# Kernel optimization log

Hardware: AMD Instinct MI355X
Metric: run time of the kernel (lower is better)

## Reference

```python
import jax, jax.numpy as jnp
import numpy as np

D_MODEL = 1024
EPS_DT = 1e-4
LN_EPS = 1e-5


def _layernorm(y, gamma, beta):
    mu = jnp.mean(y, axis=-1, keepdims=True)
    var = jnp.var(y, axis=-1, keepdims=True)
    return (y - mu) * jax.lax.rsqrt(var + LN_EPS) * gamma + beta


def setup_inputs() -> dict:
    key = jax.random.key(0)
    ks = jax.random.split(key, 8)
    B, T, D = 8, 4096, D_MODEL
    s = 1.0 / np.sqrt(D)  # ~ torch Linear default init scale
    return {
        "x": jax.random.normal(ks[0], (B, T, D), jnp.float32),
        "delta_t": jax.random.uniform(ks[1], (B, T, D), jnp.float32),
        "log_decay": jnp.zeros((D,), jnp.float32),
        "W_in": jax.random.uniform(ks[2], (D, D), jnp.float32, -s, s),
        "b_in": jax.random.uniform(ks[3], (D,), jnp.float32, -s, s),
        "W_gate": jax.random.uniform(ks[4], (D, D), jnp.float32, -s, s),
        "b_gate": jax.random.uniform(ks[5], (D,), jnp.float32, -s, s),
        "W_out": jax.random.uniform(ks[6], (D, D), jnp.float32, -s, s),
        "b_out": jax.random.uniform(ks[7], (D,), jnp.float32, -s, s),
        "gamma": jnp.ones((D,), jnp.float32),
        "beta": jnp.zeros((D,), jnp.float32),
    }


def reference(x, delta_t, log_decay, W_in, b_in, W_gate, b_gate, W_out, b_out, gamma, beta):
    B, T, D = x.shape
    decay = jax.nn.softplus(log_decay) + 1e-4          # [D]
    dt = jnp.maximum(delta_t, EPS_DT)                   # [B,T,D]
    lamb = jnp.exp(-decay * dt)                         # [B,T,D]
    # Drive terms depend only on x -> precompute in parallel (big GEMMs).
    update = jnp.einsum('btd,ed->bte', x, W_in) + b_in
    gate = jax.nn.sigmoid(jnp.einsum('btd,ed->bte', x, W_gate) + b_gate)
    drive = (1.0 - lamb) * gate * update                # [B,T,D]

    def step(state, inputs):
        l_t, d_t = inputs
        state = l_t * state + d_t
        return state, state

    state0 = jnp.zeros((B, D), x.dtype)
    final_state, states = jax.lax.scan(
        step, state0,
        (jnp.swapaxes(lamb, 0, 1), jnp.swapaxes(drive, 0, 1)))
    states = jnp.swapaxes(states, 0, 1)                 # [B,T,D]
    # dropout is identity in eval mode
    y = states + jnp.einsum('btd,ed->bte', states, W_out) + b_out
    out = _layernorm(y, gamma, beta)
    return out, final_state
```

## Files before the change

### kernel.cpp

```cpp
#include <hip/hip_runtime.h>
#include <hip/hip_bf16.h>

#define D_MODEL 1024
#define BATCH 8
#define SEQ 4096
#define MROWS (BATCH*SEQ)
#define NC 64
#define CL 64

typedef __attribute__((ext_vector_type(4))) float f32x4;
typedef __attribute__((ext_vector_type(8))) short s16x8;

__device__ __forceinline__ unsigned short f2bf(float f){
  union { float f; unsigned int u; } v; v.f = f;
  return (unsigned short)((v.u + 0x7fffu + ((v.u >> 16) & 1u)) >> 16);
}
__device__ __forceinline__ float bf2f(unsigned int bits){
  union { unsigned int u; float f; } v; v.u = bits << 16; return v.f;
}

__device__ __forceinline__ void gload16(const void* g, void* l){
  __builtin_amdgcn_global_load_lds(
      (const __attribute__((address_space(1))) unsigned int*)g,
      (__attribute__((address_space(3))) unsigned int*)l, 16, 0, 0);
}

__global__ __launch_bounds__(256)
void prep_x_kernel(const float* __restrict__ x, unsigned short* __restrict__ xb, int n4){
  int i = blockIdx.x*256 + threadIdx.x;
  int stride = gridDim.x*256;
  for (; i < n4; i += stride){
    float4 v = ((const float4*)x)[i];
    ushort4 o;
    o.x = f2bf(v.x); o.y = f2bf(v.y); o.z = f2bf(v.z); o.w = f2bf(v.w);
    ((ushort4*)xb)[i] = o;
  }
}

__global__ __launch_bounds__(256)
void prep_w_kernel(const float* __restrict__ Wi, const float* __restrict__ Wg,
                   const float* __restrict__ Wo, const float* __restrict__ ld,
                   unsigned short* __restrict__ Wib, unsigned short* __restrict__ Wgb,
                   unsigned short* __restrict__ Wob, float* __restrict__ decay){
  int i = blockIdx.x*256 + threadIdx.x;
  {
    float4 a = ((const float4*)Wi)[i]; ushort4 o;
    o.x=f2bf(a.x); o.y=f2bf(a.y); o.z=f2bf(a.z); o.w=f2bf(a.w); ((ushort4*)Wib)[i]=o;
    a = ((const float4*)Wg)[i];
    o.x=f2bf(a.x); o.y=f2bf(a.y); o.z=f2bf(a.z); o.w=f2bf(a.w); ((ushort4*)Wgb)[i]=o;
    a = ((const float4*)Wo)[i];
    o.x=f2bf(a.x); o.y=f2bf(a.y); o.z=f2bf(a.z); o.w=f2bf(a.w); ((ushort4*)Wob)[i]=o;
  }
  if (i < D_MODEL){
    float v = ld[i];
    float sp = fmaxf(v, 0.f) + log1pf(expf(-fabsf(v)));
    decay[i] = sp + 1e-4f;
  }
}

__global__ __launch_bounds__(256, 3)
void gemm1_kernel(const unsigned short* __restrict__ Aglob,
                  const unsigned short* __restrict__ Bglob,
                  const float* __restrict__ bias,
                  unsigned short* __restrict__ Cout)
{
  __shared__ unsigned short sA[128*64];
  __shared__ unsigned short sB[128*64];
  const int tid  = threadIdx.x;
  const int lane = tid & 63;
  const int wave = tid >> 6;
  const int wr = wave >> 1, wc = wave & 1;
  const int bid = blockIdx.x;
  const int swz = ((bid & 7) << 8) | (bid >> 3);
  const int bcol = (swz & 7) * 128;
  const int brow = (swz >> 3) * 128;

  const f32x4 zero = {0.f,0.f,0.f,0.f};
  f32x4 acc[4][4];
  #pragma unroll
  for (int a=0;a<4;a++)
    #pragma unroll
    for (int b=0;b<4;b++) acc[a][b]=zero;

  for (int kt = 0; kt < D_MODEL/64; ++kt){
    __syncthreads();
    #pragma unroll
    for (int i=0;i<4;i++){
      const int ob = i*256 + wave*64;
      const int o  = ob + lane;
      const int r  = o >> 3;
      const int c  = ((o & 7) ^ (r & 7)) * 16;
      gload16((const char*)Aglob + (size_t)(brow + r)*(D_MODEL*2) + (size_t)kt*128 + c,
              (char*)sA + (size_t)ob*16);
      gload16((const char*)Bglob + (size_t)(bcol + r)*(D_MODEL*2) + (size_t)kt*128 + c,
              (char*)sB + (size_t)ob*16);
    }
    __syncthreads();
    #pragma unroll
    for (int ks=0; ks<2; ++ks){
      s16x8 af[4], bf[4];
      #pragma unroll
      for (int mi=0; mi<4; mi++){
        const int row = wr*64 + mi*16 + (lane & 15);
        const int chunk = (ks*4 + (lane>>4)) ^ (row & 7);
        af[mi] = *(const s16x8*)((const char*)sA + row*128 + chunk*16);
      }
      #pragma unroll
      for (int ni=0; ni<4; ni++){
        const int n = wc*64 + ni*16 + (lane & 15);
        const int chunk = (ks*4 + (lane>>4)) ^ (n & 7);
        bf[ni] = *(const s16x8*)((const char*)sB + n*128 + chunk*16);
      }
      #pragma unroll
      for (int mi=0; mi<4; mi++)
        #pragma unroll
        for (int ni=0; ni<4; ni++)
          acc[mi][ni] = __builtin_amdgcn_mfma_f32_16x16x32_bf16(af[mi], bf[ni], acc[mi][ni], 0,0,0);
    }
  }

  #pragma unroll
  for (int ni=0; ni<4; ni++){
    const int col = bcol + wc*64 + ni*16 + (lane & 15);
    const float vb = bias[col];
    #pragma unroll
    for (int mi=0; mi<4; mi++){
      #pragma unroll
      for (int q=0; q<4; q++){
        const int row = brow + wr*64 + mi*16 + ((lane>>4)*4) + q;
        Cout[(size_t)row*D_MODEL + col] = f2bf(acc[mi][ni][q] + vb);
      }
    }
  }
}

__global__ __launch_bounds__(256)
void scan_passA(const unsigned short* __restrict__ ub,
                const unsigned short* __restrict__ gb,
                const float* __restrict__ delta,
                const float* __restrict__ decay,
                unsigned int* __restrict__ pack,
                float* __restrict__ cA, float* __restrict__ cB){
  const int d0 = (blockIdx.x*256 + threadIdx.x)*2;
  const int c = blockIdx.y, b = blockIdx.z;
  const float dc0 = decay[d0], dc1 = decay[d0+1];
  size_t base = ((size_t)b*SEQ + (size_t)c*CL)*D_MODEL + d0;
  float A0=1.f, A1=1.f, s0=0.f, s1=0.f;
  #pragma unroll 4
  for (int t=0;t<CL;t++){
    const size_t idx = base + (size_t)t*D_MODEL;
    const unsigned int uu = *(const unsigned int*)(ub + idx);
    const unsigned int gg = *(const unsigned int*)(gb + idx);
    const float2 dv = *(const float2*)(delta + idx);
    const float u0 = bf2f(uu & 0xffffu), u1 = bf2f(uu >> 16);
    const float z0 = bf2f(gg & 0xffffu), z1 = bf2f(gg >> 16);
    const float g0 = 1.f/(1.f + __expf(-z0));
    const float g1 = 1.f/(1.f + __expf(-z1));
    const float lam0 = __expf(-dc0 * fmaxf(dv.x, 1e-4f));
    const float lam1 = __expf(-dc1 * fmaxf(dv.y, 1e-4f));
    const float om0 = 1.f - lam0, om1 = 1.f - lam1;
    const float dr0 = om0 * g0 * u0;
    const float dr1 = om1 * g1 * u1;
    uint2 pw;
    pw.x = ((unsigned int)f2bf(dr0) << 16) | (unsigned int)f2bf(om0);
    pw.y = ((unsigned int)f2bf(dr1) << 16) | (unsigned int)f2bf(om1);
    *(uint2*)(pack + idx) = pw;
    A0 *= lam0; A1 *= lam1;
    s0 = fmaf(lam0, s0, dr0);
    s1 = fmaf(lam1, s1, dr1);
  }
  const size_t ci = ((size_t)b*NC + c)*D_MODEL + d0;
  *(float2*)(cA+ci) = make_float2(A0,A1);
  *(float2*)(cB+ci) = make_float2(s0,s1);
}

__global__ __launch_bounds__(256)
void scan_passB(const float* __restrict__ cA, const float* __restrict__ cB,
                float* __restrict__ cS, float* __restrict__ fstate){
  const int d0 = (blockIdx.x*256 + threadIdx.x)*2;
  const int b = blockIdx.y;
  float s0=0.f, s1=0.f;
  for (int c=0;c<NC;c++){
    const size_t ci = ((size_t)b*NC + c)*D_MODEL + d0;
    *(float2*)(cS+ci) = make_float2(s0,s1);
    float2 a  = *(const float2*)(cA+ci);
    float2 bb = *(const float2*)(cB+ci);
    s0 = fmaf(a.x, s0, bb.x);
    s1 = fmaf(a.y, s1, bb.y);
  }
  *(float2*)(fstate + (size_t)b*D_MODEL + d0) = make_float2(s0,s1);
}

__global__ __launch_bounds__(256)
void scan_passC(const unsigned int* __restrict__ pack, const float* __restrict__ cS,
                unsigned short* __restrict__ statesb){
  const int d0 = (blockIdx.x*256 + threadIdx.x)*2;
  const int c = blockIdx.y, b = blockIdx.z;
  float2 sv = *(const float2*)(cS + ((size_t)b*NC + c)*D_MODEL + d0);
  float s0 = sv.x, s1 = sv.y;
  size_t base = ((size_t)b*SEQ + (size_t)c*CL)*D_MODEL + d0;
  #pragma unroll 8
  for (int t=0;t<CL;t++){
    uint2 p = *(const uint2*)(pack + base + (size_t)t*D_MODEL);
    float om0 = bf2f(p.x & 0xffffu), dr0 = bf2f(p.x >> 16);
    float om1 = bf2f(p.y & 0xffffu), dr1 = bf2f(p.y >> 16);
    s0 = fmaf(-om0, s0, s0) + dr0;
    s1 = fmaf(-om1, s1, s1) + dr1;
    unsigned int w = ((unsigned int)f2bf(s1) << 16) | (unsigned int)f2bf(s0);
    *(unsigned int*)(statesb + base + (size_t)t*D_MODEL) = w;
  }
}

__global__ __launch_bounds__(256)
void ln_kernel(const unsigned short* __restrict__ yb, const unsigned short* __restrict__ statesb,
               const float* __restrict__ gamma, const float* __restrict__ beta,
               float* __restrict__ out)
{
  const int row = blockIdx.x;
  const int tid = threadIdx.x;
  ushort4 yv = ((const ushort4*)(yb + (size_t)row*D_MODEL))[tid];
  ushort4 sb = ((const ushort4*)(statesb + (size_t)row*D_MODEL))[tid];
  float4 v;
  v.x = bf2f(yv.x) + bf2f(sb.x);
  v.y = bf2f(yv.y) + bf2f(sb.y);
  v.z = bf2f(yv.z) + bf2f(sb.z);
  v.w = bf2f(yv.w) + bf2f(sb.w);
  float s = v.x+v.y+v.z+v.w;
  float q = v.x*v.x + v.y*v.y + v.z*v.z + v.w*v.w;
  #pragma unroll
  for (int off=32; off>0; off>>=1){ s += __shfl_xor(s, off); q += __shfl_xor(q, off); }
  __shared__ float rs[4], rq[4];
  const int wave = tid>>6, lane = tid&63;
  if (lane==0){ rs[wave]=s; rq[wave]=q; }
  __syncthreads();
  float ts = rs[0]+rs[1]+rs[2]+rs[3];
  float tq = rq[0]+rq[1]+rq[2]+rq[3];
  float mu  = ts * (1.f/D_MODEL);
  float var = tq * (1.f/D_MODEL) - mu*mu;
  float inv = rsqrtf(var + 1e-5f);
  float4 g = ((const float4*)gamma)[tid];
  float4 b = ((const float4*)beta)[tid];
  float4 o;
  o.x = (v.x-mu)*inv*g.x + b.x;
  o.y = (v.y-mu)*inv*g.y + b.y;
  o.z = (v.z-mu)*inv*g.z + b.z;
  o.w = (v.w-mu)*inv*g.w + b.w;
  ((float4*)(out + (size_t)row*D_MODEL))[tid] = o;
}

extern "C" void kernel_launch(void* const* d_in, const int* in_sizes, int n_in,
                              void* d_out, int out_size, void* d_ws, size_t ws_size,
                              hipStream_t stream) {
  const float* x         = (const float*)d_in[0];
  const float* delta     = (const float*)d_in[1];
  const float* log_decay = (const float*)d_in[2];
  const float* W_in      = (const float*)d_in[3];
  const float* b_in      = (const float*)d_in[4];
  const float* W_gate    = (const float*)d_in[5];
  const float* b_gate    = (const float*)d_in[6];
  const float* W_out     = (const float*)d_in[7];
  const float* b_out     = (const float*)d_in[8];
  const float* gamma     = (const float*)d_in[9];
  const float* beta      = (const float*)d_in[10];

  char* w = (char*)d_ws;
  unsigned short* xb   = (unsigned short*)(w);
  unsigned short* Wib  = (unsigned short*)(w + 67108864);
  unsigned short* Wgb  = (unsigned short*)(w + 69206016);
  unsigned short* Wob  = (unsigned short*)(w + 71303168);
  float*          decay= (float*)        (w + 73400320);
  float*          cA   = (float*)        (w + 73404416);
  float*          cB   = (float*)        (w + 75501568);
  float*          cS   = (float*)        (w + 77598720);
  unsigned int*   pack = (unsigned int*) (w + 79695872);
  unsigned short* ybuf = (unsigned short*)pack;
  unsigned short* statesb = xb;

  float* out    = (float*)d_out;
  float* fstate = out + (size_t)MROWS*D_MODEL;
  unsigned short* ub = (unsigned short*)d_out;
  unsigned short* gb = ub + (size_t)MROWS*D_MODEL;

  hipLaunchKernelGGL(prep_x_kernel, dim3(8192), dim3(256), 0, stream, x, xb, MROWS*D_MODEL/4);
  hipLaunchKernelGGL(prep_w_kernel, dim3(1024), dim3(256), 0, stream,
                     W_in, W_gate, W_out, log_decay, Wib, Wgb, Wob, decay);
  hipLaunchKernelGGL(gemm1_kernel, dim3(2048), dim3(256), 0, stream, xb, Wib, b_in, ub);
  hipLaunchKernelGGL(gemm1_kernel, dim3(2048), dim3(256), 0, stream, xb, Wgb, b_gate, gb);
  hipLaunchKernelGGL(scan_passA, dim3(2,NC,BATCH), dim3(256), 0, stream,
                     ub, gb, delta, decay, pack, cA, cB);
  hipLaunchKernelGGL(scan_passB, dim3(2,BATCH), dim3(256), 0, stream, cA, cB, cS, fstate);
  hipLaunchKernelGGL(scan_passC, dim3(2,NC,BATCH), dim3(256), 0, stream, pack, cS, statesb);
  hipLaunchKernelGGL(gemm1_kernel, dim3(2048), dim3(256), 0, stream, statesb, Wob, b_out, ybuf);
  hipLaunchKernelGGL(ln_kernel, dim3(MROWS), dim3(256), 0, stream, ybuf, statesb, gamma, beta, out);
}
```

Baseline: 416.6 us.

## Fuse up/gate GEMMs, merge prep kernels, fold residual into output GEMM

Merges the x and weight conversion kernels into one launch and concatenates W_in and W_gate so one GEMM with doubled N produces both update and gate, sharing A-tile loads. The output GEMM adds the residual states in-register from the A tile already staged in shared memory, so the layernorm kernel no longer rereads the states buffer. This reduces launches and global traffic, at the cost of a conditional extra LDS pass inside the GEMM loop.

```diff
diff --git a/kernel.cpp b/kernel.cpp
--- a/kernel.cpp
+++ b/kernel.cpp
@@ -26,43 +26,45 @@
 }
 
 __global__ __launch_bounds__(256)
-void prep_x_kernel(const float* __restrict__ x, unsigned short* __restrict__ xb, int n4){
-  int i = blockIdx.x*256 + threadIdx.x;
-  int stride = gridDim.x*256;
-  for (; i < n4; i += stride){
-    float4 v = ((const float4*)x)[i];
-    ushort4 o;
-    o.x = f2bf(v.x); o.y = f2bf(v.y); o.z = f2bf(v.z); o.w = f2bf(v.w);
-    ((ushort4*)xb)[i] = o;
-  }
-}
-
-__global__ __launch_bounds__(256)
-void prep_w_kernel(const float* __restrict__ Wi, const float* __restrict__ Wg,
-                   const float* __restrict__ Wo, const float* __restrict__ ld,
-                   unsigned short* __restrict__ Wib, unsigned short* __restrict__ Wgb,
-                   unsigned short* __restrict__ Wob, float* __restrict__ decay){
-  int i = blockIdx.x*256 + threadIdx.x;
-  {
+void prep_all_kernel(const float* __restrict__ x,
+                     const float* __restrict__ Wi, const float* __restrict__ Wg,
+                     const float* __restrict__ Wo, const float* __restrict__ ld,
+                     unsigned short* __restrict__ xb,
+                     unsigned short* __restrict__ Wugb,
+                     unsigned short* __restrict__ Wob,
+                     float* __restrict__ decay, int nx4){
+  const int b = blockIdx.x;
+  if (b < 8192){
+    int i = b*256 + threadIdx.x;
+    for (; i < nx4; i += 8192*256){
+      float4 v = ((const float4*)x)[i];
+      ushort4 o;
+      o.x = f2bf(v.x); o.y = f2bf(v.y); o.z = f2bf(v.z); o.w = f2bf(v.w);
+      ((ushort4*)xb)[i] = o;
+    }
+  } else {
+    const int i = (b-8192)*256 + threadIdx.x;
     float4 a = ((const float4*)Wi)[i]; ushort4 o;
-    o.x=f2bf(a.x); o.y=f2bf(a.y); o.z=f2bf(a.z); o.w=f2bf(a.w); ((ushort4*)Wib)[i]=o;
+    o.x=f2bf(a.x); o.y=f2bf(a.y); o.z=f2bf(a.z); o.w=f2bf(a.w); ((ushort4*)Wugb)[i]=o;
     a = ((const float4*)Wg)[i];
-    o.x=f2bf(a.x); o.y=f2bf(a.y); o.z=f2bf(a.z); o.w=f2bf(a.w); ((ushort4*)Wgb)[i]=o;
+    o.x=f2bf(a.x); o.y=f2bf(a.y); o.z=f2bf(a.z); o.w=f2bf(a.w); ((ushort4*)Wugb)[i + D_MODEL*D_MODEL/4]=o;
     a = ((const float4*)Wo)[i];
     o.x=f2bf(a.x); o.y=f2bf(a.y); o.z=f2bf(a.z); o.w=f2bf(a.w); ((ushort4*)Wob)[i]=o;
-  }
-  if (i < D_MODEL){
-    float v = ld[i];
-    float sp = fmaxf(v, 0.f) + log1pf(expf(-fabsf(v)));
-    decay[i] = sp + 1e-4f;
+    if (i < D_MODEL){
+      float v = ld[i];
+      float sp = fmaxf(v, 0.f) + log1pf(expf(-fabsf(v)));
+      decay[i] = sp + 1e-4f;
+    }
   }
 }
 
 __global__ __launch_bounds__(256, 3)
-void gemm1_kernel(const unsigned short* __restrict__ Aglob,
-                  const unsigned short* __restrict__ Bglob,
-                  const float* __restrict__ bias,
-                  unsigned short* __restrict__ Cout)
+void gemm_ug_kernel(const unsigned short* __restrict__ Aglob,
+                    const unsigned short* __restrict__ Bglob,
+                    const float* __restrict__ b_in,
+                    const float* __restrict__ b_gate,
+                    unsigned short* __restrict__ ub,
+                    unsigned short* __restrict__ gb)
 {
   __shared__ unsigned short sA[128*64];
   __shared__ unsigned short sB[128*64];
@@ -70,10 +72,11 @@
   const int lane = tid & 63;
   const int wave = tid >> 6;
   const int wr = wave >> 1, wc = wave & 1;
-  const int bid = blockIdx.x;
-  const int swz = ((bid & 7) << 8) | (bid >> 3);
-  const int bcol = (swz & 7) * 128;
-  const int brow = (swz >> 3) * 128;
+  const int bid  = blockIdx.x;
+  const int idx  = bid >> 3;
+  const int xcd  = bid & 7;
+  const int bcol = (idx & 15) * 128;
+  const int brow = (xcd*32 + (idx >> 4)) * 128;
 
   const f32x4 zero = {0.f,0.f,0.f,0.f};
   f32x4 acc[4][4];
@@ -119,16 +122,20 @@
     }
   }
 
+  const int half = bcol >> 10;
+  const float* bias = half ? b_gate : b_in;
+  unsigned short* Co = half ? gb : ub;
+  const int cb = bcol & 1023;
   #pragma unroll
   for (int ni=0; ni<4; ni++){
-    const int col = bcol + wc*64 + ni*16 + (lane & 15);
+    const int col = cb + wc*64 + ni*16 + (lane & 15);
     const float vb = bias[col];
     #pragma unroll
     for (int mi=0; mi<4; mi++){
       #pragma unroll
       for (int q=0; q<4; q++){
         const int row = brow + wr*64 + mi*16 + ((lane>>4)*4) + q;
-        Cout[(size_t)row*D_MODEL + col] = f2bf(acc[mi][ni][q] + vb);
+        Co[(size_t)row*D_MODEL + col] = f2bf(acc[mi][ni][q] + vb);
       }
     }
   }
@@ -211,20 +218,109 @@
   }
 }
 
-__global__ __launch_bounds__(256)
-void ln_kernel(const unsigned short* __restrict__ yb, const unsigned short* __restrict__ statesb,
+__global__ __launch_bounds__(256, 3)
+void gemm_out_kernel(const unsigned short* __restrict__ Sb,
+                     const unsigned short* __restrict__ Wob,
+                     const float* __restrict__ b_out,
+                     unsigned short* __restrict__ yb)
+{
+  __shared__ unsigned short sA[128*64];
+  __shared__ unsigned short sB[128*64];
+  const int tid  = threadIdx.x;
+  const int lane = tid & 63;
+  const int wave = tid >> 6;
+  const int wr = wave >> 1, wc = wave & 1;
+  const int bid = blockIdx.x;
+  const int swz = ((bid & 7) << 8) | (bid >> 3);
+  const int bcol = (swz & 7) * 128;
+  const int brow = (swz >> 3) * 128;
+
+  const f32x4 zero = {0.f,0.f,0.f,0.f};
+  f32x4 acc[4][4];
+  #pragma unroll
+  for (int a=0;a<4;a++)
+    #pragma unroll
+    for (int b=0;b<4;b++) acc[a][b]=zero;
+
+  const int kt_res = (bcol >> 6) + wc;
+
+  for (int kt = 0; kt < D_MODEL/64; ++kt){
+    __syncthreads();
+    #pragma unroll
+    for (int i=0;i<4;i++){
+      const int ob = i*256 + wave*64;
+      const int o  = ob + lane;
+      const int r  = o >> 3;
+      const int c  = ((o & 7) ^ (r & 7)) * 16;
+      gload16((const char*)Sb  + (size_t)(brow + r)*(D_MODEL*2) + (size_t)kt*128 + c,
+              (char*)sA + (size_t)ob*16);
+      gload16((const char*)Wob + (size_t)(bcol + r)*(D_MODEL*2) + (size_t)kt*128 + c,
+              (char*)sB + (size_t)ob*16);
+    }
+    __syncthreads();
+    #pragma unroll
+    for (int ks=0; ks<2; ++ks){
+      s16x8 af[4], bf[4];
+      #pragma unroll
+      for (int mi=0; mi<4; mi++){
+        const int row = wr*64 + mi*16 + (lane & 15);
+        const int chunk = (ks*4 + (lane>>4)) ^ (row & 7);
+        af[mi] = *(const s16x8*)((const char*)sA + row*128 + chunk*16);
+      }
+      #pragma unroll
+      for (int ni=0; ni<4; ni++){
+        const int n = wc*64 + ni*16 + (lane & 15);
+        const int chunk = (ks*4 + (lane>>4)) ^ (n & 7);
+        bf[ni] = *(const s16x8*)((const char*)sB + n*128 + chunk*16);
+      }
+      #pragma unroll
+      for (int mi=0; mi<4; mi++)
+        #pragma unroll
+        for (int ni=0; ni<4; ni++)
+          acc[mi][ni] = __builtin_amdgcn_mfma_f32_16x16x32_bf16(af[mi], bf[ni], acc[mi][ni], 0,0,0);
+    }
+    if (kt == kt_res){
+      #pragma unroll
+      for (int ni=0; ni<4; ni++){
+        #pragma unroll
+        for (int mi=0; mi<4; mi++){
+          #pragma unroll
+          for (int q=0; q<4; q++){
+            const int rl = wr*64 + mi*16 + ((lane>>4)*4) + q;
+            const int cl = ni*16 + (lane & 15);
+            const int byte = rl*128 + (((cl>>3) ^ (rl&7))*16) + ((cl&7)*2);
+            acc[mi][ni][q] += bf2f((unsigned int)*(const unsigned short*)((const char*)sA + byte));
+          }
+        }
+      }
+    }
+  }
+
+  #pragma unroll
+  for (int ni=0; ni<4; ni++){
+    const int col = bcol + wc*64 + ni*16 + (lane & 15);
+    const float vb = b_out[col];
+    #pragma unroll
+    for (int mi=0; mi<4; mi++){
+      #pragma unroll
+      for (int q=0; q<4; q++){
+        const int row = brow + wr*64 + mi*16 + ((lane>>4)*4) + q;
+        yb[(size_t)row*D_MODEL + col] = f2bf(acc[mi][ni][q] + vb);
+      }
+    }
+  }
+}
+
+__global__ __launch_bounds__(256)
+void ln_kernel(const unsigned short* __restrict__ yb,
                const float* __restrict__ gamma, const float* __restrict__ beta,
                float* __restrict__ out)
 {
   const int row = blockIdx.x;
   const int tid = threadIdx.x;
   ushort4 yv = ((const ushort4*)(yb + (size_t)row*D_MODEL))[tid];
-  ushort4 sb = ((const ushort4*)(statesb + (size_t)row*D_MODEL))[tid];
   float4 v;
-  v.x = bf2f(yv.x) + bf2f(sb.x);
-  v.y = bf2f(yv.y) + bf2f(sb.y);
-  v.z = bf2f(yv.z) + bf2f(sb.z);
-  v.w = bf2f(yv.w) + bf2f(sb.w);
+  v.x = bf2f(yv.x); v.y = bf2f(yv.y); v.z = bf2f(yv.z); v.w = bf2f(yv.w);
   float s = v.x+v.y+v.z+v.w;
   float q = v.x*v.x + v.y*v.y + v.z*v.z + v.w*v.w;
   #pragma unroll
@@ -265,8 +361,7 @@
 
   char* w = (char*)d_ws;
   unsigned short* xb   = (unsigned short*)(w);
-  unsigned short* Wib  = (unsigned short*)(w + 67108864);
-  unsigned short* Wgb  = (unsigned short*)(w + 69206016);
+  unsigned short* Wugb = (unsigned short*)(w + 67108864);
   unsigned short* Wob  = (unsigned short*)(w + 71303168);
   float*          decay= (float*)        (w + 73400320);
   float*          cA   = (float*)        (w + 73404416);
@@ -281,15 +376,15 @@
   unsigned short* ub = (unsigned short*)d_out;
   unsigned short* gb = ub + (size_t)MROWS*D_MODEL;
 
-  hipLaunchKernelGGL(prep_x_kernel, dim3(8192), dim3(256), 0, stream, x, xb, MROWS*D_MODEL/4);
-  hipLaunchKernelGGL(prep_w_kernel, dim3(1024), dim3(256), 0, stream,
-                     W_in, W_gate, W_out, log_decay, Wib, Wgb, Wob, decay);
-  hipLaunchKernelGGL(gemm1_kernel, dim3(2048), dim3(256), 0, stream, xb, Wib, b_in, ub);
-  hipLaunchKernelGGL(gemm1_kernel, dim3(2048), dim3(256), 0, stream, xb, Wgb, b_gate, gb);
+  hipLaunchKernelGGL(prep_all_kernel, dim3(9216), dim3(256), 0, stream,
+                     x, W_in, W_gate, W_out, log_decay, xb, Wugb, Wob, decay, MROWS*D_MODEL/4);
+  hipLaunchKernelGGL(gemm_ug_kernel, dim3(4096), dim3(256), 0, stream,
+                     xb, Wugb, b_in, b_gate, ub, gb);
   hipLaunchKernelGGL(scan_passA, dim3(2,NC,BATCH), dim3(256), 0, stream,
                      ub, gb, delta, decay, pack, cA, cB);
   hipLaunchKernelGGL(scan_passB, dim3(2,BATCH), dim3(256), 0, stream, cA, cB, cS, fstate);
   hipLaunchKernelGGL(scan_passC, dim3(2,NC,BATCH), dim3(256), 0, stream, pack, cS, statesb);
-  hipLaunchKernelGGL(gemm1_kernel, dim3(2048), dim3(256), 0, stream, statesb, Wob, b_out, ybuf);
-  hipLaunchKernelGGL(ln_kernel, dim3(MROWS), dim3(256), 0, stream, ybuf, statesb, gamma, beta, out);
-}
+  hipLaunchKernelGGL(gemm_out_kernel, dim3(2048), dim3(256), 0, stream,
+                     statesb, Wob, b_out, ybuf);
+  hipLaunchKernelGGL(ln_kernel, dim3(MROWS), dim3(256), 0, stream, ybuf, gamma, beta, out);
+}
```

Result: no change. 422.6 us (+1.4%).
